# Performance work log

Hardware: AMD Instinct MI355X
Metric: run time of the kernel (lower is better)

The kernel has to match this reference:

```python
import jax, jax.numpy as jnp
import numpy as np

N = 100000   # nodes
E = 1600000  # directed edges
B = 512      # graphs in batch
F = 9        # atom feature columns (OGB AtomEncoder)
V = 128      # vocab per atom feature
H = 256      # nhid
C = 10       # num_classes


def setup_inputs() -> dict:
    key = jax.random.key(0)
    ks = jax.random.split(key, 14)
    s = lambda k, shape: (jax.random.normal(k, shape, jnp.float32) * 0.05)
    return {
        "x": jax.random.randint(ks[0], (N, F), 0, V),
        "edge_index": jax.random.randint(ks[1], (2, E), 0, N),
        "batch": jnp.sort(jax.random.randint(ks[2], (N,), 0, B)),
        "atom_emb": s(ks[3], (F, V, H)),
        "W1": s(ks[4], (H, H)), "b1": s(ks[5], (H,)),
        "W2": s(ks[6], (H, H)), "b2": s(ks[7], (H,)),
        "W3": s(ks[8], (H, H)), "b3": s(ks[9], (H,)),
        "cw1": s(ks[10], (H, H // 2)), "cb1": s(ks[11], (H // 2,)),
        "cw2": s(ks[12], (H // 2, C)), "cb2": s(ks[13], (C,)),
    }


def reference(x, edge_index, batch, atom_emb, W1, b1, W2, b2, W3, b3, cw1, cb1, cw2, cb2):
    n = x.shape[0]
    # AtomEncoder: sum of per-column embeddings -> [N, H]
    h = atom_emb[jnp.arange(F)[None, :], x].sum(axis=1)

    # GCN normalization with self-loops (PyG GCNConv default)
    loop = jnp.arange(n, dtype=edge_index.dtype)
    row = jnp.concatenate([edge_index[0], loop])  # source
    col = jnp.concatenate([edge_index[1], loop])  # target
    deg = jax.ops.segment_sum(jnp.ones_like(col, jnp.float32), col, num_segments=n)
    dis = deg ** -0.5  # deg >= 1 because of self-loops
    norm = dis[row] * dis[col]  # [E+N]

    def gcn(feat, W, b):
        m = feat @ W                                   # [N, H]
        agg = jax.ops.segment_sum(norm[:, None] * m[row], col, num_segments=n)
        return agg + b

    x1 = jax.nn.relu(gcn(h, W1, b1))
    x2 = jax.nn.relu(gcn(x1, W2, b2))
    x3 = jax.nn.relu(gcn(x2, W3, b3))

    # global mean pool per graph, summed across the three layers
    counts = jax.ops.segment_sum(jnp.ones((n,), jnp.float32), batch, num_segments=B)
    pooled = jax.ops.segment_sum(x1 + x2 + x3, batch, num_segments=B) / counts[:, None]

    # classifier (dropout is identity in eval mode)
    hdn = jax.nn.relu(pooled @ cw1 + cb1)
    out = hdn @ cw2 + cb2
    return (out, 0)
```

## Files before the change

kernel.cpp:

```cpp
#include <hip/hip_runtime.h>
#include <hip/hip_bf16.h>
#include <cstdint>

#define HDIM 256
#define H2   128

using f32x4  = __attribute__((ext_vector_type(4))) float;
using bf16x8 = __attribute__((ext_vector_type(8))) short;
using u16x8  = __attribute__((ext_vector_type(8))) unsigned short;

__device__ inline unsigned short f2bf(float f) {
    unsigned x = __builtin_bit_cast(unsigned, f);
    return (unsigned short)((x + 0x7fffu + ((x >> 16) & 1u)) >> 16);
}
__device__ inline float bf2f(unsigned short u) {
    unsigned x = ((unsigned)u) << 16;
    return __builtin_bit_cast(float, x);
}

__global__ void k_init(int* __restrict__ deg, int* __restrict__ cursor,
                       float* __restrict__ pooled, int n, int bh) {
    int i = blockIdx.x * blockDim.x + threadIdx.x;
    if (i < n) { deg[i] = 1; cursor[i] = 0; }
    if (i < bh) pooled[i] = 0.f;
}

__global__ void k_deg(const int* __restrict__ col, int* __restrict__ deg, int e) {
    int i = blockIdx.x * blockDim.x + threadIdx.x;
    if (i < e) atomicAdd(&deg[col[i]], 1);
}

__global__ void k_scan1(const int* __restrict__ deg, int* __restrict__ ptr,
                        int* __restrict__ bsum, int n) {
    __shared__ int sd[256];
    int i = blockIdx.x * 256 + threadIdx.x;
    int v = (i < n) ? (deg[i] - 1) : 0;
    sd[threadIdx.x] = v;
    __syncthreads();
    for (int off = 1; off < 256; off <<= 1) {
        int t = (threadIdx.x >= off) ? sd[threadIdx.x - off] : 0;
        __syncthreads();
        sd[threadIdx.x] += t;
        __syncthreads();
    }
    if (i < n) ptr[i] = sd[threadIdx.x] - v;
    if (threadIdx.x == 255) bsum[blockIdx.x] = sd[255];
}

__global__ void k_scan2(int* __restrict__ bsum, int nb) {
    __shared__ int sd[512];
    int t = threadIdx.x;
    int v = (t < nb) ? bsum[t] : 0;
    sd[t] = v;
    __syncthreads();
    for (int off = 1; off < 512; off <<= 1) {
        int x = (t >= off) ? sd[t - off] : 0;
        __syncthreads();
        sd[t] += x;
        __syncthreads();
    }
    if (t < nb) bsum[t] = sd[t] - v;
}

__global__ void k_scan3(int* __restrict__ ptr, const int* __restrict__ bsum, int n) {
    int i = blockIdx.x * 256 + threadIdx.x;
    if (i < n) ptr[i] += bsum[blockIdx.x];
}

__global__ void k_fill(const int* __restrict__ row, const int* __restrict__ col,
                       const int* __restrict__ ptr, int* __restrict__ cursor,
                       int* __restrict__ csr_src, int e) {
    int i = blockIdx.x * blockDim.x + threadIdx.x;
    if (i < e) {
        int v = col[i];
        int s = atomicAdd(&cursor[v], 1);
        csr_src[ptr[v] + s] = row[i];
    }
}

__global__ void k_dis(const int* __restrict__ deg, float* __restrict__ dis, int n) {
    int i = blockIdx.x * blockDim.x + threadIdx.x;
    if (i < n) dis[i] = rsqrtf((float)deg[i]);
}

__global__ void k_counts(const int* __restrict__ batch, float* __restrict__ counts,
                         int n, int B) {
    int g = blockIdx.x * blockDim.x + threadIdx.x;
    if (g >= B) return;
    auto lb = [&](int key) {
        int lo = 0, hi = n;
        while (lo < hi) { int mid = (lo + hi) >> 1; if (batch[mid] < key) lo = mid + 1; else hi = mid; }
        return lo;
    };
    counts[g] = (float)(lb(g + 1) - lb(g));
}

__global__ __launch_bounds__(256) void k_atom(const int* __restrict__ x,
                                              const float* __restrict__ emb,
                                              short* __restrict__ h,
                                              int n, int F, int V) {
    int node = blockIdx.x * 4 + (threadIdx.x >> 6);
    int lane = threadIdx.x & 63;
    if (node >= n) return;
    int xv = x[node * F + (lane < F ? lane : 0)];
    float4 acc = {0.f, 0.f, 0.f, 0.f};
    for (int f = 0; f < F; ++f) {
        int idx = __shfl(xv, f, 64);
        const float4 v = *(const float4*)(emb + ((size_t)f * V + idx) * HDIM + lane * 4);
        acc.x += v.x; acc.y += v.y; acc.z += v.z; acc.w += v.w;
    }
    ushort4 o = { f2bf(acc.x), f2bf(acc.y), f2bf(acc.z), f2bf(acc.w) };
    *(ushort4*)(h + (size_t)node * HDIM + lane * 4) = o;
}

__global__ void k_wt(const float* __restrict__ W, short* __restrict__ Wt) {
    int i = blockIdx.x * 256 + threadIdx.x;
    int nn = i >> 8, k = i & 255;
    Wt[nn * HDIM + k] = (short)f2bf(W[k * HDIM + nn]);
}

__global__ __launch_bounds__(256) void k_gemm(const short* __restrict__ A,
                                              const short* __restrict__ Wt,
                                              short* __restrict__ Co, int n) {
    int wid  = threadIdx.x >> 6;
    int lane = threadIdx.x & 63;
    int wr = wid >> 1, wc = wid & 1;
    int row0 = blockIdx.x * 128 + wr * 64;
    int col0 = blockIdx.y * 128 + wc * 64;
    int lm = lane & 15;
    int kg = lane >> 4;
    f32x4 acc[4][4] = {};
    for (int kk = 0; kk < HDIM; kk += 32) {
        bf16x8 a[4], b[4];
#pragma unroll
        for (int i = 0; i < 4; ++i) {
            int r = row0 + i * 16 + lm;
            a[i] = (r < n) ? *(const bf16x8*)(A + (size_t)r * HDIM + kk + kg * 8)
                           : (bf16x8)(short)0;
        }
#pragma unroll
        for (int j = 0; j < 4; ++j) {
            int c = col0 + j * 16 + lm;
            b[j] = *(const bf16x8*)(Wt + (size_t)c * HDIM + kk + kg * 8);
        }
#pragma unroll
        for (int i = 0; i < 4; ++i)
#pragma unroll
            for (int j = 0; j < 4; ++j)
                acc[i][j] = __builtin_amdgcn_mfma_f32_16x16x32_bf16(a[i], b[j], acc[i][j], 0, 0, 0);
    }
#pragma unroll
    for (int i = 0; i < 4; ++i)
#pragma unroll
        for (int j = 0; j < 4; ++j) {
            int c = col0 + j * 16 + lm;
#pragma unroll
            for (int r4 = 0; r4 < 4; ++r4) {
                int r = row0 + i * 16 + kg * 4 + r4;
                if (r < n) Co[(size_t)r * HDIM + c] = (short)f2bf(acc[i][j][r4]);
            }
        }
}

__global__ __launch_bounds__(256) void k_agg(const short* __restrict__ mS,
                                             const int* __restrict__ csr_src,
                                             const int* __restrict__ ptr,
                                             const int* __restrict__ deg,
                                             const float* __restrict__ dis,
                                             const float* __restrict__ bias,
                                             short* __restrict__ xout, int n) {
    int node = blockIdx.x * 4 + (threadIdx.x >> 6);
    if (node >= n) return;
    int lane = threadIdx.x & 63;
    int half = lane >> 5;
    int cl = lane & 31;
    const unsigned short* m = (const unsigned short*)mS;
    float dv = dis[node];
    float acc[8] = {};
    if (half == 0) {
        u16x8 r = *(const u16x8*)(m + (size_t)node * HDIM + cl * 8);
        float sw = dv * dv;
#pragma unroll
        for (int j = 0; j < 8; ++j) acc[j] = sw * bf2f(r[j]);
    }
    int start = ptr[node];
    int cnt = deg[node] - 1;
    for (int base = 0; base < cnt; base += 64) {
        int mm = cnt - base; if (mm > 64) mm = 64;
        int uu = 0; float du = 0.f;
        if (lane < mm) {
            uu = csr_src[start + base + lane];
            du = dv * dis[uu];
        }
#pragma unroll 2
        for (int t = 0; t < 32; ++t) {
            int i = 2 * t + half;
            if (2 * t >= mm) break;
            int u   = __shfl(uu, i, 64);
            float w = __shfl(du, i, 64);
            if (i < mm) {
                u16x8 r = *(const u16x8*)(m + (size_t)u * HDIM + cl * 8);
#pragma unroll
                for (int j = 0; j < 8; ++j) acc[j] += w * bf2f(r[j]);
            }
        }
    }
#pragma unroll
    for (int j = 0; j < 8; ++j) acc[j] += __shfl_xor(acc[j], 32, 64);
    if (half == 0) {
        const float4 b0 = *(const float4*)(bias + cl * 8);
        const float4 b1 = *(const float4*)(bias + cl * 8 + 4);
        float bb[8] = {b0.x, b0.y, b0.z, b0.w, b1.x, b1.y, b1.z, b1.w};
        u16x8 o;
#pragma unroll
        for (int j = 0; j < 8; ++j)
            o[j] = f2bf(fmaxf(acc[j] + bb[j], 0.f));
        *(u16x8*)((unsigned short*)xout + (size_t)node * HDIM + cl * 8) = o;
    }
}

__global__ __launch_bounds__(256) void k_pool(const short* __restrict__ x1,
                                              const short* __restrict__ x2,
                                              const short* __restrict__ x3,
                                              const int* __restrict__ batch,
                                              float* __restrict__ pooled, int n) {
    int g = blockIdx.x, seg = blockIdx.y, t = threadIdx.x;
    auto lb = [&](int key) {
        int lo = 0, hi = n;
        while (lo < hi) { int mid = (lo + hi) >> 1; if (batch[mid] < key) lo = mid + 1; else hi = mid; }
        return lo;
    };
    int lo = lb(g), hi = lb(g + 1);
    int len = hi - lo;
    int per = (len + (int)gridDim.y - 1) / (int)gridDim.y;
    int s0 = lo + seg * per;
    int s1 = s0 + per; if (s1 > hi) s1 = hi;
    float acc = 0.f;
    for (int r = s0; r < s1; ++r) {
        size_t base = (size_t)r * HDIM + t;
        acc += bf2f((unsigned short)x1[base]) + bf2f((unsigned short)x2[base])
             + bf2f((unsigned short)x3[base]);
    }
    if (s0 < s1) atomicAdd(&pooled[g * HDIM + t], acc);
}

__global__ __launch_bounds__(H2) void k_cls(const float* __restrict__ pooled,
                                            const float* __restrict__ counts,
                                            const float* __restrict__ cw1,
                                            const float* __restrict__ cb1,
                                            const float* __restrict__ cw2,
                                            const float* __restrict__ cb2,
                                            float* __restrict__ out, int B, int C) {
    __shared__ float sp[HDIM];
    __shared__ float sh[H2];
    int g = blockIdx.x, t = threadIdx.x;
    float inv = 1.0f / counts[g];
    sp[t] = pooled[g * HDIM + t] * inv;
    sp[t + H2] = pooled[g * HDIM + t + H2] * inv;
    __syncthreads();
    float acc = cb1[t];
    for (int h = 0; h < HDIM; ++h) acc += sp[h] * cw1[h * H2 + t];
    sh[t] = fmaxf(acc, 0.f);
    __syncthreads();
    if (t < C) {
        float o = cb2[t];
        for (int j = 0; j < H2; ++j) o += sh[j] * cw2[j * C + t];
        out[g * C + t] = o;
    }
    if (g == 0 && t == 0) out[B * C] = 0.f;
}

extern "C" void kernel_launch(void* const* d_in, const int* in_sizes, int n_in,
                              void* d_out, int out_size, void* d_ws, size_t ws_size,
                              hipStream_t stream) {
    const int* x      = (const int*)d_in[0];
    const int* erow   = (const int*)d_in[1];
    const int* batch  = (const int*)d_in[2];
    const float* emb  = (const float*)d_in[3];
    const float* W1   = (const float*)d_in[4];
    const float* b1   = (const float*)d_in[5];
    const float* W2   = (const float*)d_in[6];
    const float* b2   = (const float*)d_in[7];
    const float* W3   = (const float*)d_in[8];
    const float* b3   = (const float*)d_in[9];
    const float* cw1  = (const float*)d_in[10];
    const float* cb1  = (const float*)d_in[11];
    const float* cw2  = (const float*)d_in[12];
    const float* cb2  = (const float*)d_in[13];
    float* out = (float*)d_out;

    const int N = in_sizes[2];
    const int E = in_sizes[1] / 2;
    const int F = in_sizes[0] / N;
    const int V = in_sizes[3] / (F * HDIM);
    const int C = in_sizes[13];
    const int B = (out_size - 1) / C;
    const int* ecol = erow + E;

    char* w = (char*)d_ws;
    auto carve = [&](size_t bytes) {
        void* p = (void*)w;
        w += (bytes + 255) & ~(size_t)255;
        return p;
    };
    short* P0     = (short*)carve((size_t)N * HDIM * 2);
    short* P1     = (short*)carve((size_t)N * HDIM * 2);
    short* P2     = (short*)carve((size_t)N * HDIM * 2);
    short* mS     = (short*)carve((size_t)N * HDIM * 2);
    short* Wt1    = (short*)carve((size_t)HDIM * HDIM * 2);
    short* Wt2    = (short*)carve((size_t)HDIM * HDIM * 2);
    short* Wt3    = (short*)carve((size_t)HDIM * HDIM * 2);
    float* dis    = (float*)carve((size_t)N * 4);
    float* pooled = (float*)carve((size_t)B * HDIM * 4);
    float* counts = (float*)carve((size_t)B * 4);
    int* deg      = (int*)carve((size_t)N * 4);
    int* ptr      = (int*)carve((size_t)N * 4);
    int* cursor   = (int*)carve((size_t)N * 4);
    int* bsum     = (int*)carve(1024 * 4);
    int* csr      = (int*)carve((size_t)E * 4);

    int nblk = (N + 255) / 256;
    int initspan = (B * HDIM > N) ? B * HDIM : N;

    k_init<<<(initspan + 255) / 256, 256, 0, stream>>>(deg, cursor, pooled, N, B * HDIM);
    k_deg<<<(E + 255) / 256, 256, 0, stream>>>(ecol, deg, E);
    k_scan1<<<nblk, 256, 0, stream>>>(deg, ptr, bsum, N);
    k_scan2<<<1, 512, 0, stream>>>(bsum, nblk);
    k_scan3<<<nblk, 256, 0, stream>>>(ptr, bsum, N);
    k_fill<<<(E + 255) / 256, 256, 0, stream>>>(erow, ecol, ptr, cursor, csr, E);
    k_dis<<<nblk, 256, 0, stream>>>(deg, dis, N);
    k_counts<<<(B + 255) / 256, 256, 0, stream>>>(batch, counts, N, B);
    k_wt<<<HDIM, 256, 0, stream>>>(W1, Wt1);
    k_wt<<<HDIM, 256, 0, stream>>>(W2, Wt2);
    k_wt<<<HDIM, 256, 0, stream>>>(W3, Wt3);
    k_atom<<<(N + 3) / 4, 256, 0, stream>>>(x, emb, P0, N, F, V);

    dim3 ggrid((N + 127) / 128, 2);
    int agrid = (N + 3) / 4;

    k_gemm<<<ggrid, 256, 0, stream>>>(P0, Wt1, mS, N);
    k_agg<<<agrid, 256, 0, stream>>>(mS, csr, ptr, deg, dis, b1, P1, N);
    k_gemm<<<ggrid, 256, 0, stream>>>(P1, Wt2, mS, N);
    k_agg<<<agrid, 256, 0, stream>>>(mS, csr, ptr, deg, dis, b2, P2, N);
    k_gemm<<<ggrid, 256, 0, stream>>>(P2, Wt3, mS, N);
    k_agg<<<agrid, 256, 0, stream>>>(mS, csr, ptr, deg, dis, b3, P0, N);

    dim3 pgrid(B, 4);
    k_pool<<<pgrid, 256, 0, stream>>>(P1, P2, P0, batch, pooled, N);
    k_cls<<<B, H2, 0, stream>>>(pooled, counts, cw1, cb1, cw2, cb2, out, B, C);
}
```

Baseline: 835.6 us.

## Fuse small setup kernels, widen GEMM tile to full width, batch gather loads in aggregation

Folds the rsqrt degree computation into the scan finalisation and merges the three weight-transpose launches into one 2D launch, cutting launch count. The GEMM now gives each block all 256 output columns (each wave 128 columns, 32 accumulators), so A rows are read once instead of twice, at the cost of higher register pressure. The aggregation loop issues four neighbour-row gathers before accumulating, raising memory-level parallelism, and uses a nontemporal load for CSR indices. Invalid slots load row 0 with zero weight instead of branching.

```diff
diff --git a/kernel.cpp b/kernel.cpp
--- a/kernel.cpp
+++ b/kernel.cpp
@@ -62,9 +62,13 @@
     if (t < nb) bsum[t] = sd[t] - v;
 }
 
-__global__ void k_scan3(int* __restrict__ ptr, const int* __restrict__ bsum, int n) {
+__global__ void k_scan3(int* __restrict__ ptr, const int* __restrict__ bsum,
+                        const int* __restrict__ deg, float* __restrict__ dis, int n) {
     int i = blockIdx.x * 256 + threadIdx.x;
-    if (i < n) ptr[i] += bsum[blockIdx.x];
+    if (i < n) {
+        ptr[i] += bsum[blockIdx.x];
+        dis[i] = rsqrtf((float)deg[i]);
+    }
 }
 
 __global__ void k_fill(const int* __restrict__ row, const int* __restrict__ col,
@@ -76,11 +80,6 @@
         int s = atomicAdd(&cursor[v], 1);
         csr_src[ptr[v] + s] = row[i];
     }
-}
-
-__global__ void k_dis(const int* __restrict__ deg, float* __restrict__ dis, int n) {
-    int i = blockIdx.x * blockDim.x + threadIdx.x;
-    if (i < n) dis[i] = rsqrtf((float)deg[i]);
 }
 
 __global__ void k_counts(const int* __restrict__ batch, float* __restrict__ counts,
@@ -113,7 +112,11 @@
     *(ushort4*)(h + (size_t)node * HDIM + lane * 4) = o;
 }
 
-__global__ void k_wt(const float* __restrict__ W, short* __restrict__ Wt) {
+__global__ void k_wt3(const float* __restrict__ W1, const float* __restrict__ W2,
+                      const float* __restrict__ W3, short* __restrict__ Wt1,
+                      short* __restrict__ Wt2, short* __restrict__ Wt3) {
+    const float* W = (blockIdx.y == 0) ? W1 : (blockIdx.y == 1) ? W2 : W3;
+    short* Wt      = (blockIdx.y == 0) ? Wt1 : (blockIdx.y == 1) ? Wt2 : Wt3;
     int i = blockIdx.x * 256 + threadIdx.x;
     int nn = i >> 8, k = i & 255;
     Wt[nn * HDIM + k] = (short)f2bf(W[k * HDIM + nn]);
@@ -126,12 +129,12 @@
     int lane = threadIdx.x & 63;
     int wr = wid >> 1, wc = wid & 1;
     int row0 = blockIdx.x * 128 + wr * 64;
-    int col0 = blockIdx.y * 128 + wc * 64;
+    int col0 = wc * 128;
     int lm = lane & 15;
     int kg = lane >> 4;
-    f32x4 acc[4][4] = {};
+    f32x4 acc[4][8] = {};
     for (int kk = 0; kk < HDIM; kk += 32) {
-        bf16x8 a[4], b[4];
+        bf16x8 a[4], b[8];
 #pragma unroll
         for (int i = 0; i < 4; ++i) {
             int r = row0 + i * 16 + lm;
@@ -139,20 +142,20 @@
                            : (bf16x8)(short)0;
         }
 #pragma unroll
-        for (int j = 0; j < 4; ++j) {
+        for (int j = 0; j < 8; ++j) {
             int c = col0 + j * 16 + lm;
             b[j] = *(const bf16x8*)(Wt + (size_t)c * HDIM + kk + kg * 8);
         }
 #pragma unroll
         for (int i = 0; i < 4; ++i)
 #pragma unroll
-            for (int j = 0; j < 4; ++j)
+            for (int j = 0; j < 8; ++j)
                 acc[i][j] = __builtin_amdgcn_mfma_f32_16x16x32_bf16(a[i], b[j], acc[i][j], 0, 0, 0);
     }
 #pragma unroll
     for (int i = 0; i < 4; ++i)
 #pragma unroll
-        for (int j = 0; j < 4; ++j) {
+        for (int j = 0; j < 8; ++j) {
             int c = col0 + j * 16 + lm;
 #pragma unroll
             for (int r4 = 0; r4 < 4; ++r4) {
@@ -189,20 +192,25 @@
         int mm = cnt - base; if (mm > 64) mm = 64;
         int uu = 0; float du = 0.f;
         if (lane < mm) {
-            uu = csr_src[start + base + lane];
-            du = dv * dis[uu];
-        }
-#pragma unroll 2
-        for (int t = 0; t < 32; ++t) {
-            int i = 2 * t + half;
-            if (2 * t >= mm) break;
-            int u   = __shfl(uu, i, 64);
-            float w = __shfl(du, i, 64);
-            if (i < mm) {
-                u16x8 r = *(const u16x8*)(m + (size_t)u * HDIM + cl * 8);
-#pragma unroll
-                for (int j = 0; j < 8; ++j) acc[j] += w * bf2f(r[j]);
+            uu = __builtin_nontemporal_load(&csr_src[start + base + lane]);
+            du = dis[uu];
+        }
+        int nst = (mm + 7) >> 3;
+        for (int s = 0; s < nst; ++s) {
+            u16x8 r[4]; float w[4];
+#pragma unroll
+            for (int q = 0; q < 4; ++q) {
+                int i = 8 * s + 2 * q + half;
+                int u   = __shfl(uu, i & 63, 64);
+                float ww = dv * __shfl(du, i & 63, 64);
+                bool v = i < mm;
+                w[q] = v ? ww : 0.f;
+                r[q] = *(const u16x8*)(m + (size_t)(v ? u : 0) * HDIM + cl * 8);
             }
+#pragma unroll
+            for (int q = 0; q < 4; ++q)
+#pragma unroll
+                for (int j = 0; j < 8; ++j) acc[j] += w[q] * bf2f(r[q][j]);
         }
     }
 #pragma unroll
@@ -326,16 +334,14 @@
     k_deg<<<(E + 255) / 256, 256, 0, stream>>>(ecol, deg, E);
     k_scan1<<<nblk, 256, 0, stream>>>(deg, ptr, bsum, N);
     k_scan2<<<1, 512, 0, stream>>>(bsum, nblk);
-    k_scan3<<<nblk, 256, 0, stream>>>(ptr, bsum, N);
+    k_scan3<<<nblk, 256, 0, stream>>>(ptr, bsum, deg, dis, N);
     k_fill<<<(E + 255) / 256, 256, 0, stream>>>(erow, ecol, ptr, cursor, csr, E);
-    k_dis<<<nblk, 256, 0, stream>>>(deg, dis, N);
     k_counts<<<(B + 255) / 256, 256, 0, stream>>>(batch, counts, N, B);
-    k_wt<<<HDIM, 256, 0, stream>>>(W1, Wt1);
-    k_wt<<<HDIM, 256, 0, stream>>>(W2, Wt2);
-    k_wt<<<HDIM, 256, 0, stream>>>(W3, Wt3);
+    dim3 wgrid(HDIM, 3);
+    k_wt3<<<wgrid, 256, 0, stream>>>(W1, W2, W3, Wt1, Wt2, Wt3);
     k_atom<<<(N + 3) / 4, 256, 0, stream>>>(x, emb, P0, N, F, V);
 
-    dim3 ggrid((N + 127) / 128, 2);
+    int ggrid = (N + 127) / 128;
     int agrid = (N + 3) / 4;
 
     k_gemm<<<ggrid, 256, 0, stream>>>(P0, Wt1, mS, N);
```

Result: no change. 838.4 us, median of 2 (+0.3%).
